# Kernel tuning notes

Hardware: AMD Instinct MI355X
Metric: run time of the kernel (lower is better)

Reference implementation:

```python
import jax, jax.numpy as jnp
import numpy as np
from jax import lax
import math

B, C, H, W = 8, 512, 24, 24
L = H * W
D_STATE = 16
D_INNER = 2 * C
DT_RANK = C // 16
K = 4
SCALE = 1.0 / math.sqrt(C)


def layer_norm(x, g, b, eps=1e-5):
    m = x.mean(-1, keepdims=True)
    v = ((x - m) ** 2).mean(-1, keepdims=True)
    return (x - m) * lax.rsqrt(v + eps) * g + b


def selective_scan(u, delta, A, Bm, Cm, Ds):
    # u, delta: (B,K,d,L); Bm, Cm: (B,K,N,L); A: (K,d,N); Ds: (K,d)
    us = jnp.moveaxis(u, -1, 0)      # (L,B,K,d)
    dts = jnp.moveaxis(delta, -1, 0)
    Bs = jnp.moveaxis(Bm, -1, 0)     # (L,B,K,N)
    Cs = jnp.moveaxis(Cm, -1, 0)

    def step(h, inp):
        u_t, dt_t, B_t, C_t = inp
        dA = jnp.exp(dt_t[..., None] * A)                      # (B,K,d,N)
        dBu = (dt_t * u_t)[..., None] * B_t[:, :, None, :]     # (B,K,d,N)
        h = dA * h + dBu
        y = jnp.einsum('bkdn,bkn->bkd', h, C_t)
        return h, y

    h0 = jnp.zeros(u.shape[:3] + (A.shape[-1],), u.dtype)
    _, ys = lax.scan(step, h0, (us, dts, Bs, Cs))
    y = jnp.moveaxis(ys, 0, -1)                                # (B,K,d,L)
    return y + Ds[None, :, :, None] * u


def ss2d(x, in_proj_w, dwconv_w, dwconv_b, x_proj_w, dt_proj_w, dt_proj_b,
         A_logs, Ds, out_norm_g, out_norm_b, out_proj_w):
    # x: (B,H,W,C) channel-last
    xz = x @ in_proj_w.T                                       # (B,H,W,2*d_inner)
    xi, z = jnp.split(xz, 2, axis=-1)
    xc = xi.transpose(0, 3, 1, 2)                              # (B,d_inner,H,W)
    xc = lax.conv_general_dilated(xc, dwconv_w, (1, 1), 'SAME',
                                  feature_group_count=D_INNER,
                                  dimension_numbers=('NCHW', 'OIHW', 'NCHW'))
    xc = jax.nn.silu(xc + dwconv_b[None, :, None, None])
    x_hw = xc.reshape(B, D_INNER, L)
    x_wh = xc.transpose(0, 1, 3, 2).reshape(B, D_INNER, L)
    xs = jnp.stack([x_hw, x_wh, x_hw[..., ::-1], x_wh[..., ::-1]], axis=1)  # (B,4,d,L)
    x_dbl = jnp.einsum('bkdl,kcd->bkcl', xs, x_proj_w)
    dt, Bm, Cm = jnp.split(x_dbl, [DT_RANK, DT_RANK + D_STATE], axis=2)
    delta = jax.nn.softplus(jnp.einsum('bkrl,kdr->bkdl', dt, dt_proj_w)
                            + dt_proj_b[None, :, :, None])
    A = -jnp.exp(A_logs)
    ys = selective_scan(xs, delta, A, Bm, Cm, Ds)              # (B,4,d,L)
    y_wh = ys[:, 1].reshape(B, D_INNER, W, H).transpose(0, 1, 3, 2).reshape(B, D_INNER, L)
    y_whr = ys[:, 3, :, ::-1].reshape(B, D_INNER, W, H).transpose(0, 1, 3, 2).reshape(B, D_INNER, L)
    y = ys[:, 0] + ys[:, 2, :, ::-1] + y_wh + y_whr
    y = y.reshape(B, D_INNER, H, W).transpose(0, 2, 3, 1)      # (B,H,W,d_inner)
    y = layer_norm(y, out_norm_g, out_norm_b)
    y = y * jax.nn.silu(z)
    return y @ out_proj_w.T                                    # (B,H,W,C)


def setup_inputs():
    key = jax.random.key(0)
    ks = jax.random.split(key, 10)
    n = lambda k, sh, s=0.02: jax.random.normal(k, sh, dtype=jnp.float32) * s
    return {
        'x5': jax.random.normal(ks[0], (B, C, H, W), dtype=jnp.float32),
        'conv_w': n(ks[1], (C, C)),
        'conv_b': jnp.zeros((C,), jnp.float32),
        'ln1_g': jnp.ones((C,), jnp.float32),
        'ln1_b': jnp.zeros((C,), jnp.float32),
        'in_proj_w': n(ks[2], (2 * D_INNER, C)),
        'dwconv_w': n(ks[3], (D_INNER, 1, 3, 3), 0.1),
        'dwconv_b': jnp.zeros((D_INNER,), jnp.float32),
        'x_proj_w': n(ks[4], (K, DT_RANK + 2 * D_STATE, D_INNER)),
        'dt_proj_w': n(ks[5], (K, D_INNER, DT_RANK), 0.1),
        'dt_proj_b': n(ks[6], (K, D_INNER), 0.1),
        'A_logs': jnp.tile(jnp.log(jnp.arange(1, D_STATE + 1, dtype=jnp.float32))[None, None, :],
                           (K, D_INNER, 1)),
        'Ds': jnp.ones((K, D_INNER), jnp.float32),
        'out_norm_g': jnp.ones((D_INNER,), jnp.float32),
        'out_norm_b': jnp.zeros((D_INNER,), jnp.float32),
        'out_proj_w': n(ks[7], (C, D_INNER)),
    }


def reference(x5, conv_w, conv_b, ln1_g, ln1_b, in_proj_w, dwconv_w, dwconv_b,
              x_proj_w, dt_proj_w, dt_proj_b, A_logs, Ds, out_norm_g, out_norm_b,
              out_proj_w):
    # 1x1 conv + residual
    x5 = jnp.einsum('bchw,oc->bohw', x5, conv_w) + conv_b[None, :, None, None] + x5
    x0 = x5.transpose(0, 2, 3, 1)                              # (B,H,W,C)
    # VSSBlock: x + SS2D(LN(x)); called twice on same input with same weights -> identical
    x00 = x0 + ss2d(layer_norm(x0, ln1_g, ln1_b), in_proj_w, dwconv_w, dwconv_b,
                    x_proj_w, dt_proj_w, dt_proj_b, A_logs, Ds,
                    out_norm_g, out_norm_b, out_proj_w)
    xq = x00.transpose(0, 3, 1, 2).reshape(B, C, L)            # (B,C,L)
    xq_flat = xq.transpose(0, 2, 1).reshape(B * L, C)          # (B*L, C)
    xk_flat = xq.transpose(1, 0, 2).reshape(C, B * L)          # (C, B*L)
    xw = (xq_flat @ xk_flat) * SCALE                           # (B*L, B*L)
    xw = xw.reshape(B * L, B, L).max(-1).mean(-1).reshape(B, L)
    xw = jax.nn.softmax(xw, axis=-1)
    norm0 = x5 / jnp.maximum(jnp.linalg.norm(x5, axis=1, keepdims=True), 1e-12)
    xw = xw[:, None, :]                                        # (B,1,L)
    xw_max = xw.max(-1, keepdims=True)
    mask = (xw == xw_max).astype(x5.dtype).reshape(B, 1, H, W)  # winner-take-all
    seeds = (norm0 * mask).sum((2, 3))                         # (B,C)
    # correlation (eval branch: relu), seeds act as 1x1 conv weights
    cor = jax.nn.relu(jnp.einsum('bchw,oc->bohw', norm0, seeds)).mean(1).reshape(B, L)
    mn = cor.min(1, keepdims=True)
    mx = cor.max(1, keepdims=True)
    cormap = ((cor - mn) / (mx - mn + 1e-12)).reshape(B, 1, H, W)
    x51 = x5 * cormap
    proto1 = x51.mean((0, 2, 3), keepdims=True)                # (1,C,1,1)
    return (x5, proto1, x5 * proto1 + x51, mask)
```

## Files before the change

### kernel.cpp

```cpp
#include <hip/hip_runtime.h>
#include <math.h>

#define NB 8
#define NC 512
#define NH 24
#define NW 24
#define NL 576
#define ND 1024
#define NBL 4608
#define NCH 8
#define CL 72

static constexpr float SCALE_ = 0.044194173824159216f;

typedef __attribute__((ext_vector_type(8))) short bf16x8;
typedef __attribute__((ext_vector_type(4))) float f32x4;

__device__ __forceinline__ unsigned enc_f(float f){
    unsigned u = __float_as_uint(f);
    return (u & 0x80000000u) ? ~u : (u | 0x80000000u);
}
__device__ __forceinline__ float dec_f(unsigned e){
    return (e & 0x80000000u) ? __uint_as_float(e ^ 0x80000000u) : __uint_as_float(~e);
}

__device__ __forceinline__ int scan_idx(int t, int k){
    int t2 = (k >= 2) ? (NL - 1 - t) : t;
    return (k & 1) ? ((t2 % NH) * NW + t2 / NH) : t2;
}

__device__ __forceinline__ float softplus_f(float x){
    return fmaxf(x, 0.f) + __logf(1.f + __expf(-fabsf(x)));
}
__device__ __forceinline__ float silu_f(float x){
    return x / (1.f + __expf(-x));
}

__global__ void k_transpose_in(const float* __restrict__ x5, float* __restrict__ x5t){
    __shared__ float t[32][33];
    const int b = blockIdx.z;
    const int c0 = blockIdx.x*32, l0 = blockIdx.y*32;
    const int tx = threadIdx.x & 31, ty = threadIdx.x >> 5;
    #pragma unroll
    for (int i=ty; i<32; i+=8)
        t[i][tx] = x5[((size_t)b*NC + c0 + i)*NL + l0 + tx];
    __syncthreads();
    #pragma unroll
    for (int i=ty; i<32; i+=8)
        x5t[((size_t)b*NL + l0 + i)*NC + c0 + tx] = t[tx][i];
}

template<int FORM>
__global__ void k_split(const float* __restrict__ in, unsigned short* __restrict__ oA,
                        unsigned short* __restrict__ oB, int K, int total4){
    int t = blockIdx.x*256 + threadIdx.x;
    if (t >= total4) return;
    int kq = K >> 2;
    int r = t / kq; int k4 = (t - r*kq) << 2;
    float4 v = *(const float4*)(in + (size_t)r*K + k4);
    float vv[4] = {v.x, v.y, v.z, v.w};
    unsigned short h[4], lo[4];
    #pragma unroll
    for (int i=0;i<4;i++){
        unsigned u = __float_as_uint(vv[i]);
        unsigned hr = (u + 0x7fffu + ((u>>16)&1u)) >> 16;
        h[i] = (unsigned short)hr;
        float hf = __uint_as_float(hr << 16);
        unsigned u2 = __float_as_uint(vv[i] - hf);
        lo[i] = (unsigned short)((u2 + 0x7fffu + ((u2>>16)&1u)) >> 16);
    }
    unsigned hp0 = h[0] | ((unsigned)h[1]<<16), hp1 = h[2] | ((unsigned)h[3]<<16);
    unsigned lp0 = lo[0] | ((unsigned)lo[1]<<16), lp1 = lo[2] | ((unsigned)lo[3]<<16);
    size_t base = (size_t)r*3*K + k4;
    if (FORM == 0 || FORM == 2){
        unsigned* p0 = (unsigned*)(oA + base);
        unsigned* p1 = (unsigned*)(oA + base + K);
        unsigned* p2 = (unsigned*)(oA + base + 2*K);
        p0[0]=hp0; p0[1]=hp1;  p1[0]=hp0; p1[1]=hp1;  p2[0]=lp0; p2[1]=lp1;
    }
    if (FORM == 1 || FORM == 2){
        unsigned short* o = (FORM==2) ? oB : oA;
        unsigned* p0 = (unsigned*)(o + base);
        unsigned* p1 = (unsigned*)(o + base + K);
        unsigned* p2 = (unsigned*)(o + base + 2*K);
        p0[0]=hp0; p0[1]=hp1;  p1[0]=lp0; p1[1]=lp1;  p2[0]=hp0; p2[1]=hp1;
    }
}

template<int MODE>
__launch_bounds__(256)
__global__ void mfma_nt(const unsigned short* __restrict__ A, const unsigned short* __restrict__ Bm,
                        const float* __restrict__ R0, const float* __restrict__ R1,
                        float* __restrict__ out0, float* __restrict__ out1,
                        unsigned* __restrict__ mbuf, int K3)
{
    const int bi = blockIdx.x, bj = blockIdx.y;
    if (MODE == 4 && bj < bi) return;
    const int m0 = bi*128, n0 = bj*128;
    __shared__ __align__(16) unsigned short As[128*32];
    __shared__ __align__(16) unsigned short Bs[128*32];
    const int tid = threadIdx.x;
    const int w = tid >> 6, l = tid & 63;
    const int mw = (w>>1)*64, nw = (w&1)*64;
    const int fr = l & 15, fq = l >> 4;

    f32x4 acc[4][4];
    #pragma unroll
    for (int i=0;i<4;i++)
        #pragma unroll
        for (int j=0;j<4;j++)
            #pragma unroll
            for (int c=0;c<4;c++) acc[i][j][c] = 0.f;

    const int c0 = tid, c1 = tid + 256;
    const int r0 = c0 >> 2, o0 = (c0 & 3) * 8;
    const int r1 = c1 >> 2, o1 = (c1 & 3) * 8;

    for (int k0 = 0; k0 < K3; k0 += 32){
        float4 a0 = *(const float4*)(A  + (size_t)(m0 + r0)*K3 + k0 + o0);
        float4 a1 = *(const float4*)(A  + (size_t)(m0 + r1)*K3 + k0 + o1);
        float4 b0 = *(const float4*)(Bm + (size_t)(n0 + r0)*K3 + k0 + o0);
        float4 b1 = *(const float4*)(Bm + (size_t)(n0 + r1)*K3 + k0 + o1);
        __syncthreads();
        *(float4*)&As[c0*8] = a0;
        *(float4*)&As[c1*8] = a1;
        *(float4*)&Bs[c0*8] = b0;
        *(float4*)&Bs[c1*8] = b1;
        __syncthreads();
        bf16x8 af[4], bf[4];
        #pragma unroll
        for (int i=0;i<4;i++){
            af[i] = *(const bf16x8*)&As[(mw + i*16 + fr)*32 + fq*8];
            bf[i] = *(const bf16x8*)&Bs[(nw + i*16 + fr)*32 + fq*8];
        }
        #pragma unroll
        for (int i=0;i<4;i++)
            #pragma unroll
            for (int j=0;j<4;j++)
                acc[i][j] = __builtin_amdgcn_mfma_f32_16x16x32_bf16(af[i], bf[j], acc[i][j], 0, 0, 0);
    }

    if (MODE == 4){
        const int b2c = (n0 + nw) / NL;
        #pragma unroll
        for (int mi=0; mi<4; mi++){
            #pragma unroll
            for (int i=0;i<4;i++){
                float v = fmaxf(fmaxf(acc[mi][0][i], acc[mi][1][i]),
                                fmaxf(acc[mi][2][i], acc[mi][3][i]));
                v = fmaxf(v, __shfl_xor(v, 1));
                v = fmaxf(v, __shfl_xor(v, 2));
                v = fmaxf(v, __shfl_xor(v, 4));
                v = fmaxf(v, __shfl_xor(v, 8));
                if (fr == 0)
                    atomicMax(&mbuf[(size_t)(m0 + mw + mi*16 + fq*4 + i)*NB + b2c], enc_f(v));
            }
        }
        const int b2r = (m0 + mw) / NL;
        #pragma unroll
        for (int ni=0; ni<4; ni++){
            float cm = -3.4e38f;
            #pragma unroll
            for (int mi=0; mi<4; mi++)
                #pragma unroll
                for (int i=0;i<4;i++) cm = fmaxf(cm, acc[mi][ni][i]);
            cm = fmaxf(cm, __shfl_xor(cm, 16));
            cm = fmaxf(cm, __shfl_xor(cm, 32));
            if (fq == 0)
                atomicMax(&mbuf[(size_t)(n0 + nw + ni*16 + fr)*NB + b2r], enc_f(cm));
        }
        return;
    }

    #pragma unroll
    for (int mi=0; mi<4; mi++){
        const int m = m0 + mw + mi*16 + fq*4;
        #pragma unroll
        for (int ni=0; ni<4; ni++){
            const int n = n0 + nw + ni*16 + fr;
            f32x4 a = acc[mi][ni];
            if (MODE == 0){
                float4 cb = *(const float4*)(R0 + m);
                float4 rs = *(const float4*)(R1 + (size_t)n*NC + m);
                float4 ov = make_float4(a[0]+cb.x+rs.x, a[1]+cb.y+rs.y, a[2]+cb.z+rs.z, a[3]+cb.w+rs.w);
                *(float4*)(out0 + (size_t)n*NC + m) = ov;
            } else if (MODE == 1){
                float4 ov = make_float4(a[0], a[1], a[2], a[3]);
                if (m < ND) *(float4*)(out0 + (size_t)n*ND + m) = ov;
                else        *(float4*)(out1 + (size_t)n*ND + (m - ND)) = ov;
            } else {
                float4 rs = *(const float4*)(R1 + (size_t)n*NC + m);
                float4 ov = make_float4(a[0]+rs.x, a[1]+rs.y, a[2]+rs.z, a[3]+rs.w);
                *(float4*)(out0 + (size_t)n*NC + m) = ov;
            }
        }
    }
}

template<int MODE>
__launch_bounds__(256)
__global__ void gemm_nt(const float* __restrict__ A0, const float* __restrict__ B0,
                        const float* __restrict__ R,
                        float* __restrict__ out0, float* __restrict__ out1,
                        unsigned* __restrict__ mbuf, int K)
{
    __shared__ __align__(16) float As[16][68];
    __shared__ __align__(16) float Bs[16][68];
    const int tid = threadIdx.x;
    const int m0 = blockIdx.x * 64;
    const int n0 = blockIdx.y * 64;
    const float* A = A0;
    const float* B = B0;
    int kdir = 0;
    if (MODE == 2) {
        const int bk = blockIdx.z;
        kdir = bk & 3; const int bb = bk >> 2;
        A = A0 + (size_t)kdir * 64 * 1024;
        B = B0 + (size_t)bb * NL * 1024;
    }
    const int lrow = tid >> 2;
    const int lk4  = (tid & 3) << 2;
    int brow = n0 + lrow;
    if (MODE == 2) brow = scan_idx(brow, kdir);
    const float* aptr = A + (size_t)(m0 + lrow) * K + lk4;
    const float* bptr = B + (size_t)brow * K + lk4;

    float acc[4][4];
    #pragma unroll
    for (int i=0;i<4;i++){
        #pragma unroll
        for (int j=0;j<4;j++) acc[i][j]=0.f;
    }
    const int tx = tid & 15, ty = tid >> 4;

    for (int k0 = 0; k0 < K; k0 += 16) {
        float4 av = *(const float4*)(aptr + k0);
        float4 bv = *(const float4*)(bptr + k0);
        __syncthreads();
        As[lk4+0][lrow]=av.x; As[lk4+1][lrow]=av.y; As[lk4+2][lrow]=av.z; As[lk4+3][lrow]=av.w;
        Bs[lk4+0][lrow]=bv.x; Bs[lk4+1][lrow]=bv.y; Bs[lk4+2][lrow]=bv.z; Bs[lk4+3][lrow]=bv.w;
        __syncthreads();
        #pragma unroll
        for (int kk=0;kk<16;kk++){
            float4 a = *(const float4*)&As[kk][ty<<2];
            float4 b = *(const float4*)&Bs[kk][tx<<2];
            acc[0][0] = fmaf(a.x,b.x,acc[0][0]); acc[0][1] = fmaf(a.x,b.y,acc[0][1]);
            acc[0][2] = fmaf(a.x,b.z,acc[0][2]); acc[0][3] = fmaf(a.x,b.w,acc[0][3]);
            acc[1][0] = fmaf(a.y,b.x,acc[1][0]); acc[1][1] = fmaf(a.y,b.y,acc[1][1]);
            acc[1][2] = fmaf(a.y,b.z,acc[1][2]); acc[1][3] = fmaf(a.y,b.w,acc[1][3]);
            acc[2][0] = fmaf(a.z,b.x,acc[2][0]); acc[2][1] = fmaf(a.z,b.y,acc[2][1]);
            acc[2][2] = fmaf(a.z,b.z,acc[2][2]); acc[2][3] = fmaf(a.z,b.w,acc[2][3]);
            acc[3][0] = fmaf(a.w,b.x,acc[3][0]); acc[3][1] = fmaf(a.w,b.y,acc[3][1]);
            acc[3][2] = fmaf(a.w,b.z,acc[3][2]); acc[3][3] = fmaf(a.w,b.w,acc[3][3]);
        }
    }

    #pragma unroll
    for (int j=0;j<4;j++){
        const int n  = n0 + (tx<<2) + j;
        const int mm = m0 + (ty<<2);
        float4 v = make_float4(acc[0][j], acc[1][j], acc[2][j], acc[3][j]);
        if (MODE == 2){
            *(float4*)(out0 + ((size_t)blockIdx.z*NL + n)*64 + mm) = v;
        }
    }
}

__global__ void k_ln512(const float* __restrict__ x, const float* __restrict__ g,
                        const float* __restrict__ bb, float* __restrict__ out){
    int n = blockIdx.x; int tid = threadIdx.x;
    const float* row = x + (size_t)n*NC;
    float v0 = row[tid], v1 = row[tid+256];
    __shared__ float s1[256], s2[256];
    s1[tid] = v0+v1; s2[tid] = v0*v0 + v1*v1;
    __syncthreads();
    for (int s=128;s>0;s>>=1){ if (tid<s){ s1[tid]+=s1[tid+s]; s2[tid]+=s2[tid+s]; } __syncthreads(); }
    float mean = s1[0]*(1.f/NC);
    float var  = fmaxf(s2[0]*(1.f/NC) - mean*mean, 0.f);
    float rs   = rsqrtf(var + 1e-5f);
    out[(size_t)n*NC+tid]     = (v0-mean)*rs*g[tid]     + bb[tid];
    out[(size_t)n*NC+tid+256] = (v1-mean)*rs*g[tid+256] + bb[tid+256];
}

__global__ void k_dwconv(const float* __restrict__ xi, const float* __restrict__ w,
                         const float* __restrict__ bias, float* __restrict__ xcl){
    int d = blockIdx.x*256 + threadIdx.x;
    int l = blockIdx.y; int b = blockIdx.z;
    int h = l / NW, wc = l - h*NW;
    float acc = bias[d];
    #pragma unroll
    for (int kh=0;kh<3;kh++){
        int h2 = h + kh - 1; if (h2 < 0 || h2 >= NH) continue;
        #pragma unroll
        for (int kw=0;kw<3;kw++){
            int w2 = wc + kw - 1; if (w2 < 0 || w2 >= NW) continue;
            acc += xi[((size_t)b*NL + h2*NW + w2)*ND + d] * w[d*9 + kh*3 + kw];
        }
    }
    xcl[((size_t)b*NL + l)*ND + d] = silu_f(acc);
}

__launch_bounds__(256)
__global__ void k_scan_p1(const float* __restrict__ xcl, const float* __restrict__ xdbl,
                          const float* __restrict__ dtw, const float* __restrict__ dtb,
                          const float* __restrict__ alogs,
                          float* __restrict__ hfin, float* __restrict__ prodA){
    const int d = blockIdx.x*256 + threadIdx.x;
    const int chunk = blockIdx.y;
    const int bk = blockIdx.z;
    const int k = bk & 3, b = bk >> 2;
    const int kd = k*ND + d;
    float wdt[32];
    {
        const float4* p = (const float4*)(dtw + (size_t)kd*32);
        #pragma unroll
        for (int i=0;i<8;i++){ float4 v=p[i]; wdt[4*i]=v.x; wdt[4*i+1]=v.y; wdt[4*i+2]=v.z; wdt[4*i+3]=v.w; }
    }
    float An[16];
    {
        const float4* p = (const float4*)(alogs + (size_t)kd*16);
        #pragma unroll
        for (int i=0;i<4;i++){
            float4 v=p[i];
            An[4*i]=-__expf(v.x); An[4*i+1]=-__expf(v.y); An[4*i+2]=-__expf(v.z); An[4*i+3]=-__expf(v.w);
        }
    }
    const float dtbias = dtb[kd];
    __shared__ __align__(16) float rows[CL*64];
    {
        const float4* src = (const float4*)(xdbl + ((size_t)bk*NL + chunk*CL)*64);
        for (int i = threadIdx.x; i < CL*16; i += 256) ((float4*)rows)[i] = src[i];
    }
    __syncthreads();
    float h[16], pA[16];
    #pragma unroll
    for (int n=0;n<16;n++){ h[n]=0.f; pA[n]=1.f; }
    for (int t=0;t<CL;t++){
        const float* row = rows + t*64;
        float dr = dtbias;
        #pragma unroll
        for (int r=0;r<32;r++) dr = fmaf(row[r], wdt[r], dr);
        float sp = softplus_f(dr);
        int idx = scan_idx(chunk*CL + t, k);
        float u  = xcl[((size_t)b*NL + idx)*ND + d];
        float du = sp * u;
        #pragma unroll
        for (int n=0;n<16;n++){
            float dA = __expf(sp * An[n]);
            pA[n] *= dA;
            h[n] = fmaf(dA, h[n], du*row[32+n]);
        }
    }
    size_t base = (size_t)(bk*NCH + chunk)*16*1024 + d;
    #pragma unroll
    for (int n=0;n<16;n++){ hfin[base + n*1024] = h[n]; prodA[base + n*1024] = pA[n]; }
}

__global__ void k_scan_mid(float* __restrict__ hfin, const float* __restrict__ prodA){
    int id = blockIdx.x*256 + threadIdx.x;
    int d = id & 1023, nn = (id >> 10) & 15, bk = id >> 14;
    float h = 0.f;
    for (int j=0;j<NCH;j++){
        size_t idx = (size_t)((bk*NCH + j)*16 + nn)*1024 + d;
        float hf = hfin[idx], pa = prodA[idx];
        hfin[idx] = h;
        h = fmaf(pa, h, hf);
    }
}

__launch_bounds__(256)
__global__ void k_scan_p2(const float* __restrict__ xcl, const float* __restrict__ xdbl,
                          const float* __restrict__ dtw, const float* __restrict__ dtb,
                          const float* __restrict__ alogs,
                          const float* __restrict__ hfin, float* __restrict__ yacc){
    const int d = blockIdx.x*256 + threadIdx.x;
    const int chunk = blockIdx.y;
    const int bk = blockIdx.z;
    const int k = bk & 3, b = bk >> 2;
    const int kd = k*ND + d;
    float wdt[32];
    {
        const float4* p = (const float4*)(dtw + (size_t)kd*32);
        #pragma unroll
        for (int i=0;i<8;i++){ float4 v=p[i]; wdt[4*i]=v.x; wdt[4*i+1]=v.y; wdt[4*i+2]=v.z; wdt[4*i+3]=v.w; }
    }
    float An[16];
    {
        const float4* p = (const float4*)(alogs + (size_t)kd*16);
        #pragma unroll
        for (int i=0;i<4;i++){
            float4 v=p[i];
            An[4*i]=-__expf(v.x); An[4*i+1]=-__expf(v.y); An[4*i+2]=-__expf(v.z); An[4*i+3]=-__expf(v.w);
        }
    }
    const float dtbias = dtb[kd];
    __shared__ __align__(16) float rows[CL*64];
    {
        const float4* src = (const float4*)(xdbl + ((size_t)bk*NL + chunk*CL)*64);
        for (int i = threadIdx.x; i < CL*16; i += 256) ((float4*)rows)[i] = src[i];
    }
    __syncthreads();
    float h[16];
    {
        size_t base = (size_t)(bk*NCH + chunk)*16*1024 + d;
        #pragma unroll
        for (int n=0;n<16;n++) h[n] = hfin[base + n*1024];
    }
    for (int t=0;t<CL;t++){
        const float* row = rows + t*64;
        float dr = dtbias;
        #pragma unroll
        for (int r=0;r<32;r++) dr = fmaf(row[r], wdt[r], dr);
        float sp = softplus_f(dr);
        int idx = scan_idx(chunk*CL + t, k);
        size_t base = ((size_t)b*NL + idx)*ND + d;
        float u  = xcl[base];
        float du = sp * u;
        float y = 0.f;
        #pragma unroll
        for (int n=0;n<16;n++){
            float dA = __expf(sp * An[n]);
            h[n] = fmaf(dA, h[n], du*row[32+n]);
            y = fmaf(h[n], row[48+n], y);
        }
        atomicAdd(&yacc[base], y);
    }
}

__global__ void k_combine(const float* __restrict__ y, const float* __restrict__ xcl,
                          const float* __restrict__ Ds,
                          const float* __restrict__ g, const float* __restrict__ bb,
                          float* __restrict__ z){
    int n = blockIdx.x;
    size_t base = (size_t)n*ND;
    int tid = threadIdx.x;
    float v[4]; float sum=0.f, sq=0.f;
    #pragma unroll
    for (int j=0;j<4;j++){
        int d = tid + 256*j;
        float ds = Ds[d] + Ds[ND+d] + Ds[2*ND+d] + Ds[3*ND+d];
        float val = y[base+d] + ds*xcl[base+d];
        v[j]=val; sum+=val; sq+=val*val;
    }
    __shared__ float s1[256], s2[256];
    s1[tid]=sum; s2[tid]=sq; __syncthreads();
    for (int st=128;st>0;st>>=1){ if(tid<st){ s1[tid]+=s1[tid+st]; s2[tid]+=s2[tid+st]; } __syncthreads(); }
    float mean = s1[0]*(1.f/ND);
    float var  = fmaxf(s2[0]*(1.f/ND) - mean*mean, 0.f);
    float rs   = rsqrtf(var + 1e-5f);
    #pragma unroll
    for (int j=0;j<4;j++){
        int d = tid + 256*j;
        float ln = (v[j]-mean)*rs*g[d] + bb[d];
        float zv = z[base+d];
        z[base+d] = ln * silu_f(zv);
    }
}

__global__ void k_xwpre(const unsigned* __restrict__ M, float* __restrict__ xwp){
    int n = blockIdx.x*256 + threadIdx.x; if (n >= NBL) return;
    float sum = 0.f;
    #pragma unroll
    for (int b2=0;b2<NB;b2++) sum += dec_f(M[(size_t)n*NB + b2]);
    xwp[n] = sum * (SCALE_/8.f);
}

__global__ void k_mask(const float* __restrict__ xwp, float* __restrict__ maskf){
    int b = blockIdx.x; int tid = threadIdx.x;
    float m = -1e30f;
    for (int i=tid;i<NL;i+=64) m = fmaxf(m, xwp[b*NL+i]);
    __shared__ float s1[64];
    s1[tid]=m; __syncthreads();
    for (int st=32;st>0;st>>=1){ if(tid<st) s1[tid]=fmaxf(s1[tid],s1[tid+st]); __syncthreads(); }
    float bm = s1[0];
    for (int i=tid;i<NL;i+=64) maskf[b*NL+i] = (xwp[b*NL+i]==bm) ? 1.f : 0.f;
}

__global__ void k_norm0(const float* __restrict__ x5r, float* __restrict__ norm0){
    int n = blockIdx.x; int tid = threadIdx.x;
    float v0 = x5r[(size_t)n*NC+tid], v1 = x5r[(size_t)n*NC+tid+256];
    __shared__ float s1[256];
    s1[tid] = v0*v0 + v1*v1; __syncthreads();
    for (int st=128;st>0;st>>=1){ if(tid<st) s1[tid]+=s1[tid+st]; __syncthreads(); }
    float inv = 1.f / fmaxf(sqrtf(s1[0]), 1e-12f);
    norm0[(size_t)n*NC+tid]     = v0*inv;
    norm0[(size_t)n*NC+tid+256] = v1*inv;
}

__global__ void k_seeds(const float* __restrict__ norm0, const float* __restrict__ maskf,
                        float* __restrict__ seeds){
    int b = blockIdx.x; int c = threadIdx.x;
    float acc = 0.f;
    for (int l=0;l<NL;l++){
        float mk = maskf[b*NL+l];
        if (mk != 0.f) acc += norm0[((size_t)b*NL+l)*NC + c]*mk;
    }
    seeds[b*NC + c] = acc;
}

__global__ void k_cor(const float* __restrict__ norm0, const float* __restrict__ seeds,
                      float* __restrict__ cor){
    int n = blockIdx.x; int tid = threadIdx.x;
    int o = tid >> 6, lane = tid & 63;
    float acc = 0.f;
    #pragma unroll
    for (int i=0;i<8;i++){
        int c = lane + 64*i;
        acc += norm0[(size_t)n*NC + c] * seeds[o*NC + c];
    }
    #pragma unroll
    for (int s=32;s>0;s>>=1) acc += __shfl_xor(acc, s);
    __shared__ float sr[8];
    if (lane == 0) sr[o] = fmaxf(acc, 0.f);
    __syncthreads();
    if (tid == 0){
        float r = 0.f;
        #pragma unroll
        for (int o2=0;o2<8;o2++) r += sr[o2];
        cor[n] = r * (1.f/8.f);
    }
}

__global__ void k_cormap(const float* __restrict__ cor, float* __restrict__ cmap){
    int b = blockIdx.x, tid = threadIdx.x;
    float mn = 1e30f, mx = -1e30f;
    for (int i=tid;i<NL;i+=64){ float v=cor[b*NL+i]; mn=fminf(mn,v); mx=fmaxf(mx,v); }
    __shared__ float sn[64], sx[64];
    sn[tid]=mn; sx[tid]=mx; __syncthreads();
    for (int st=32;st>0;st>>=1){ if(tid<st){ sn[tid]=fminf(sn[tid],sn[tid+st]); sx[tid]=fmaxf(sx[tid],sx[tid+st]); } __syncthreads(); }
    float MN=sn[0], MX=sx[0];
    float inv = 1.f/(MX-MN+1e-12f);
    for (int i=tid;i<NL;i+=64) cmap[b*NL+i] = (cor[b*NL+i]-MN)*inv;
}

__global__ void k_proto(const float* __restrict__ x5r, const float* __restrict__ cmap,
                        float* __restrict__ pacc){
    int c = threadIdx.x;
    int chunk = blockIdx.x;
    float acc = 0.f;
    for (int i=0;i<64;i++){
        int n = chunk*64 + i;
        acc += x5r[(size_t)n*NC + c] * cmap[n];
    }
    atomicAdd(&pacc[c], acc);
}

__global__ void k_final(const float* __restrict__ x5r, const float* __restrict__ cmap,
                        const float* __restrict__ pacc, const float* __restrict__ maskf,
                        float* __restrict__ out){
    int id = blockIdx.x*256 + threadIdx.x;
    int l = id % NL; int bc = id / NL; int c = bc & 511; int b = bc >> 9;
    float v  = x5r[((size_t)b*NL + l)*NC + c];
    float p  = pacc[c] * (1.f/(float)NBL);
    float cm = cmap[b*NL + l];
    out[id] = v;
    out[2359296 + 512 + id] = v*(p + cm);
    if (id < 512)  out[2359296 + id] = pacc[id] * (1.f/(float)NBL);
    if (id < NBL)  out[2359296 + 512 + 2359296 + id] = maskf[id];
}

extern "C" void kernel_launch(void* const* d_in, const int* in_sizes, int n_in,
                              void* d_out, int out_size, void* d_ws, size_t ws_size,
                              hipStream_t stream) {
    const float* x5        = (const float*)d_in[0];
    const float* conv_w    = (const float*)d_in[1];
    const float* conv_b    = (const float*)d_in[2];
    const float* ln1_g     = (const float*)d_in[3];
    const float* ln1_b     = (const float*)d_in[4];
    const float* in_proj_w = (const float*)d_in[5];
    const float* dwconv_w  = (const float*)d_in[6];
    const float* dwconv_b  = (const float*)d_in[7];
    const float* x_proj_w  = (const float*)d_in[8];
    const float* dt_proj_w = (const float*)d_in[9];
    const float* dt_proj_b = (const float*)d_in[10];
    const float* A_logs    = (const float*)d_in[11];
    const float* Ds        = (const float*)d_in[12];
    const float* out_norm_g= (const float*)d_in[13];
    const float* out_norm_b= (const float*)d_in[14];
    const float* out_proj_w= (const float*)d_in[15];

    float* ws = (float*)d_ws;
    const size_t O_X5R  = 0;
    const size_t O_XLN  = 2359296;
    const size_t O_XI   = 4718592;
    const size_t O_Z    = 9437184;
    const size_t O_XCL  = 14155776;
    const size_t O_XDBL = 18874368;
    const size_t O_HF   = 20054016;
    const size_t O_PA   = 24248320;
    const size_t O_MBUF = 28442624;
    const size_t O_XWP  = 28479488;
    const size_t O_MASK = 28484096;
    const size_t O_COR  = 28488704;
    const size_t O_CMAP = 28493312;
    const size_t O_SEED = 28497920;
    const size_t O_PACC = 28502016;

    float* x5r  = ws + O_X5R;
    float* xln  = ws + O_XLN;
    float* xqf  = ws + O_XLN;
    float* xi   = ws + O_XI;
    float* yacc = ws + O_XI;
    unsigned short* wAo = (unsigned short*)(ws + O_XI);
    float* z    = ws + O_Z;
    float* xcl  = ws + O_XCL;
    unsigned short* wAi = (unsigned short*)(ws + O_XCL);
    float* nrm0 = ws + O_XCL;
    float* xdbl = ws + O_XDBL;
    float* x5t  = ws + O_HF;
    float* hfin = ws + O_HF;
    unsigned short* xlnB = (unsigned short*)(ws + O_HF);
    unsigned short* zB   = (unsigned short*)(ws + O_HF);
    unsigned short* xqfA = (unsigned short*)(ws + O_HF);
    float* prodA = ws + O_PA;
    unsigned short* x5tB = (unsigned short*)(ws + O_PA);
    unsigned short* wAc  = (unsigned short*)(ws + O_PA) + 7077888;
    unsigned short* xqfB = (unsigned short*)(ws + O_PA);
    unsigned* mbuf = (unsigned*)(ws + O_MBUF);
    float* xwp  = ws + O_XWP;
    float* maskf= ws + O_MASK;
    float* cor  = ws + O_COR;
    float* cmap = ws + O_CMAP;
    float* seeds= ws + O_SEED;
    float* pacc = ws + O_PACC;

    hipMemsetAsync(mbuf, 0, 36864*sizeof(unsigned), stream);
    hipMemsetAsync(pacc, 0, 512*sizeof(float), stream);

    k_transpose_in<<<dim3(16,18,8), 256, 0, stream>>>(x5, x5t);
    k_split<0><<<256, 256, 0, stream>>>(conv_w, wAc, nullptr, 512, 65536);
    k_split<1><<<2304, 256, 0, stream>>>(x5t, x5tB, nullptr, 512, 589824);
    mfma_nt<0><<<dim3(4,36), 256, 0, stream>>>(wAc, x5tB, conv_b, x5t, x5r, nullptr, nullptr, 1536);
    k_ln512<<<NBL, 256, 0, stream>>>(x5r, ln1_g, ln1_b, xln);
    k_split<0><<<1024, 256, 0, stream>>>(in_proj_w, wAi, nullptr, 512, 262144);
    k_split<1><<<2304, 256, 0, stream>>>(xln, xlnB, nullptr, 512, 589824);
    mfma_nt<1><<<dim3(16,36), 256, 0, stream>>>(wAi, xlnB, nullptr, nullptr, xi, z, nullptr, 1536);
    k_dwconv<<<dim3(4,NL,NB), 256, 0, stream>>>(xi, dwconv_w, dwconv_b, xcl);
    hipMemsetAsync(yacc, 0, (size_t)4718592*sizeof(float), stream);
    gemm_nt<2><<<dim3(1,9,32), 256, 0, stream>>>(x_proj_w, xcl, nullptr, xdbl, nullptr, nullptr, 1024);
    k_scan_p1<<<dim3(4,NCH,32), 256, 0, stream>>>(xcl, xdbl, dt_proj_w, dt_proj_b, A_logs, hfin, prodA);
    k_scan_mid<<<2048, 256, 0, stream>>>(hfin, prodA);
    k_scan_p2<<<dim3(4,NCH,32), 256, 0, stream>>>(xcl, xdbl, dt_proj_w, dt_proj_b, A_logs, hfin, yacc);
    k_combine<<<NBL, 256, 0, stream>>>(yacc, xcl, Ds, out_norm_g, out_norm_b, z);
    k_split<1><<<4608, 256, 0, stream>>>(z, zB, nullptr, 1024, 1179648);
    k_split<0><<<512, 256, 0, stream>>>(out_proj_w, wAo, nullptr, 1024, 131072);
    mfma_nt<3><<<dim3(4,36), 256, 0, stream>>>(wAo, zB, nullptr, x5r, xqf, nullptr, nullptr, 3072);
    k_split<2><<<2304, 256, 0, stream>>>(xqf, xqfA, xqfB, 512, 589824);
    mfma_nt<4><<<dim3(36,36), 256, 0, stream>>>(xqfA, xqfB, nullptr, nullptr, nullptr, nullptr, mbuf, 1536);
    k_xwpre<<<18, 256, 0, stream>>>(mbuf, xwp);
    k_mask<<<NB, 64, 0, stream>>>(xwp, maskf);
    k_norm0<<<NBL, 256, 0, stream>>>(x5r, nrm0);
    k_seeds<<<NB, 512, 0, stream>>>(nrm0, maskf, seeds);
    k_cor<<<NBL, 512, 0, stream>>>(nrm0, seeds, cor);
    k_cormap<<<NB, 64, 0, stream>>>(cor, cmap);
    k_proto<<<72, 512, 0, stream>>>(x5r, cmap, pacc);
    k_final<<<9216, 256, 0, stream>>>(x5r, cmap, pacc, maskf, (float*)d_out);
}
```

Measured before the change: 752.6 us.

## Fuse bf16 splits into producers, slide dwconv window, use exp power ladder in scan

Folds the hi/lo bf16 splitting into the transpose, layernorm and combine kernels, removing three standalone split passes and their intermediate fp32 writes. The depthwise conv now has each thread walk a whole row with a register sliding window, cutting redundant loads. The scans detect at runtime when A equals -(n+1) and replace 16 exps per step with one exp plus multiplies. This adds a branch and a small rounding difference from repeated products.

```diff
diff --git a/kernel.cpp b/kernel.cpp
--- a/kernel.cpp
+++ b/kernel.cpp
@@ -36,7 +36,17 @@
     return x / (1.f + __expf(-x));
 }
 
-__global__ void k_transpose_in(const float* __restrict__ x5, float* __restrict__ x5t){
+__device__ __forceinline__ void split_bf(float v, unsigned short &h, unsigned short &l){
+    unsigned u = __float_as_uint(v);
+    unsigned hr = (u + 0x7fffu + ((u>>16)&1u)) >> 16;
+    h = (unsigned short)hr;
+    float hf = __uint_as_float(hr << 16);
+    unsigned u2 = __float_as_uint(v - hf);
+    l = (unsigned short)((u2 + 0x7fffu + ((u2>>16)&1u)) >> 16);
+}
+
+__global__ void k_transpose_in(const float* __restrict__ x5, float* __restrict__ x5t,
+                               unsigned short* __restrict__ x5tB){
     __shared__ float t[32][33];
     const int b = blockIdx.z;
     const int c0 = blockIdx.x*32, l0 = blockIdx.y*32;
@@ -46,8 +56,13 @@
         t[i][tx] = x5[((size_t)b*NC + c0 + i)*NL + l0 + tx];
     __syncthreads();
     #pragma unroll
-    for (int i=ty; i<32; i+=8)
-        x5t[((size_t)b*NL + l0 + i)*NC + c0 + tx] = t[tx][i];
+    for (int i=ty; i<32; i+=8){
+        float v = t[tx][i];
+        x5t[((size_t)b*NL + l0 + i)*NC + c0 + tx] = v;
+        unsigned short hh, ll; split_bf(v, hh, ll);
+        size_t rb = ((size_t)b*NL + l0 + i)*1536 + c0 + tx;
+        x5tB[rb] = hh; x5tB[rb+512] = ll; x5tB[rb+1024] = hh;
+    }
 }
 
 template<int FORM>
@@ -61,14 +76,7 @@
     float vv[4] = {v.x, v.y, v.z, v.w};
     unsigned short h[4], lo[4];
     #pragma unroll
-    for (int i=0;i<4;i++){
-        unsigned u = __float_as_uint(vv[i]);
-        unsigned hr = (u + 0x7fffu + ((u>>16)&1u)) >> 16;
-        h[i] = (unsigned short)hr;
-        float hf = __uint_as_float(hr << 16);
-        unsigned u2 = __float_as_uint(vv[i] - hf);
-        lo[i] = (unsigned short)((u2 + 0x7fffu + ((u2>>16)&1u)) >> 16);
-    }
+    for (int i=0;i<4;i++) split_bf(vv[i], h[i], lo[i]);
     unsigned hp0 = h[0] | ((unsigned)h[1]<<16), hp1 = h[2] | ((unsigned)h[3]<<16);
     unsigned lp0 = lo[0] | ((unsigned)lo[1]<<16), lp1 = lo[2] | ((unsigned)lo[3]<<16);
     size_t base = (size_t)r*3*K + k4;
@@ -266,8 +274,8 @@
     }
 }
 
-__global__ void k_ln512(const float* __restrict__ x, const float* __restrict__ g,
-                        const float* __restrict__ bb, float* __restrict__ out){
+__global__ void k_ln512b(const float* __restrict__ x, const float* __restrict__ g,
+                         const float* __restrict__ bb, unsigned short* __restrict__ outB){
     int n = blockIdx.x; int tid = threadIdx.x;
     const float* row = x + (size_t)n*NC;
     float v0 = row[tid], v1 = row[tid+256];
@@ -278,27 +286,51 @@
     float mean = s1[0]*(1.f/NC);
     float var  = fmaxf(s2[0]*(1.f/NC) - mean*mean, 0.f);
     float rs   = rsqrtf(var + 1e-5f);
-    out[(size_t)n*NC+tid]     = (v0-mean)*rs*g[tid]     + bb[tid];
-    out[(size_t)n*NC+tid+256] = (v1-mean)*rs*g[tid+256] + bb[tid+256];
+    float r0 = (v0-mean)*rs*g[tid]     + bb[tid];
+    float r1 = (v1-mean)*rs*g[tid+256] + bb[tid+256];
+    unsigned short h0,l0,h1,l1; split_bf(r0,h0,l0); split_bf(r1,h1,l1);
+    size_t base = (size_t)n*1536;
+    outB[base+tid]     =h0; outB[base+512+tid]     =l0; outB[base+1024+tid]     =h0;
+    outB[base+tid+256] =h1; outB[base+512+tid+256] =l1; outB[base+1024+tid+256] =h1;
 }
 
 __global__ void k_dwconv(const float* __restrict__ xi, const float* __restrict__ w,
                          const float* __restrict__ bias, float* __restrict__ xcl){
     int d = blockIdx.x*256 + threadIdx.x;
-    int l = blockIdx.y; int b = blockIdx.z;
-    int h = l / NW, wc = l - h*NW;
-    float acc = bias[d];
-    #pragma unroll
-    for (int kh=0;kh<3;kh++){
-        int h2 = h + kh - 1; if (h2 < 0 || h2 >= NH) continue;
-        #pragma unroll
-        for (int kw=0;kw<3;kw++){
-            int w2 = wc + kw - 1; if (w2 < 0 || w2 >= NW) continue;
-            acc += xi[((size_t)b*NL + h2*NW + w2)*ND + d] * w[d*9 + kh*3 + kw];
-        }
-    }
-    xcl[((size_t)b*NL + l)*ND + d] = silu_f(acc);
-}
+    int h = blockIdx.y; int b = blockIdx.z;
+    float W[9];
+    #pragma unroll
+    for (int i=0;i<9;i++) W[i] = w[d*9+i];
+    float bs = bias[d];
+    const size_t rb = ((size_t)b*NL)*ND + d;
+    const bool hm = h > 0, hp = h < NH-1;
+    float p0=0.f,p1=0.f,p2=0.f;
+    float c0 = hm ? xi[rb + (size_t)((h-1)*NW)*ND] : 0.f;
+    float c1 = xi[rb + (size_t)(h*NW)*ND];
+    float c2 = hp ? xi[rb + (size_t)((h+1)*NW)*ND] : 0.f;
+    for (int wc=0; wc<NW; wc++){
+        float n0,n1,n2;
+        if (wc < NW-1){
+            n0 = hm ? xi[rb + (size_t)((h-1)*NW+wc+1)*ND] : 0.f;
+            n1 = xi[rb + (size_t)(h*NW+wc+1)*ND];
+            n2 = hp ? xi[rb + (size_t)((h+1)*NW+wc+1)*ND] : 0.f;
+        } else { n0=0.f;n1=0.f;n2=0.f; }
+        float acc = bs;
+        acc = fmaf(W[0],p0, fmaf(W[1],c0, fmaf(W[2],n0, acc)));
+        acc = fmaf(W[3],p1, fmaf(W[4],c1, fmaf(W[5],n1, acc)));
+        acc = fmaf(W[6],p2, fmaf(W[7],c2, fmaf(W[8],n2, acc)));
+        xcl[rb + (size_t)(h*NW+wc)*ND] = silu_f(acc);
+        p0=c0;p1=c1;p2=c2; c0=n0;c1=n1;c2=n2;
+    }
+}
+
+#define DA_POWERS \
+    float e1=__expf(-sp); float e2=e1*e1; float e3=e2*e1; float e4=e2*e2; \
+    float e6=e4*e2; float e7=e4*e3; float e8=e4*e4; float e12=e8*e4; \
+    float dA[16]; \
+    dA[0]=e1; dA[1]=e2; dA[2]=e3; dA[3]=e4; dA[4]=e4*e1; dA[5]=e6; dA[6]=e7; dA[7]=e8; \
+    dA[8]=e8*e1; dA[9]=e8*e2; dA[10]=e8*e3; dA[11]=e12; dA[12]=e12*e1; dA[13]=e12*e2; \
+    dA[14]=e12*e3; dA[15]=e8*e8;
 
 __launch_bounds__(256)
 __global__ void k_scan_p1(const float* __restrict__ xcl, const float* __restrict__ xdbl,
@@ -316,7 +348,7 @@
         #pragma unroll
         for (int i=0;i<8;i++){ float4 v=p[i]; wdt[4*i]=v.x; wdt[4*i+1]=v.y; wdt[4*i+2]=v.z; wdt[4*i+3]=v.w; }
     }
-    float An[16];
+    float An[16]; bool ladder = true;
     {
         const float4* p = (const float4*)(alogs + (size_t)kd*16);
         #pragma unroll
@@ -324,6 +356,8 @@
             float4 v=p[i];
             An[4*i]=-__expf(v.x); An[4*i+1]=-__expf(v.y); An[4*i+2]=-__expf(v.z); An[4*i+3]=-__expf(v.w);
         }
+        #pragma unroll
+        for (int n=0;n<16;n++) ladder = ladder && (fabsf(An[n] + (float)(n+1)) < 1e-3f*(n+1));
     }
     const float dtbias = dtb[kd];
     __shared__ __align__(16) float rows[CL*64];
@@ -335,20 +369,39 @@
     float h[16], pA[16];
     #pragma unroll
     for (int n=0;n<16;n++){ h[n]=0.f; pA[n]=1.f; }
-    for (int t=0;t<CL;t++){
-        const float* row = rows + t*64;
-        float dr = dtbias;
-        #pragma unroll
-        for (int r=0;r<32;r++) dr = fmaf(row[r], wdt[r], dr);
-        float sp = softplus_f(dr);
-        int idx = scan_idx(chunk*CL + t, k);
-        float u  = xcl[((size_t)b*NL + idx)*ND + d];
-        float du = sp * u;
-        #pragma unroll
-        for (int n=0;n<16;n++){
-            float dA = __expf(sp * An[n]);
-            pA[n] *= dA;
-            h[n] = fmaf(dA, h[n], du*row[32+n]);
+    if (ladder){
+        for (int t=0;t<CL;t++){
+            const float* row = rows + t*64;
+            float dr = dtbias;
+            #pragma unroll
+            for (int r=0;r<32;r++) dr = fmaf(row[r], wdt[r], dr);
+            float sp = softplus_f(dr);
+            int idx = scan_idx(chunk*CL + t, k);
+            float u  = xcl[((size_t)b*NL + idx)*ND + d];
+            float du = sp * u;
+            DA_POWERS
+            #pragma unroll
+            for (int n=0;n<16;n++){
+                pA[n] *= dA[n];
+                h[n] = fmaf(dA[n], h[n], du*row[32+n]);
+            }
+        }
+    } else {
+        for (int t=0;t<CL;t++){
+            const float* row = rows + t*64;
+            float dr = dtbias;
+            #pragma unroll
+            for (int r=0;r<32;r++) dr = fmaf(row[r], wdt[r], dr);
+            float sp = softplus_f(dr);
+            int idx = scan_idx(chunk*CL + t, k);
+            float u  = xcl[((size_t)b*NL + idx)*ND + d];
+            float du = sp * u;
+            #pragma unroll
+            for (int n=0;n<16;n++){
+                float dA = __expf(sp * An[n]);
+                pA[n] *= dA;
+                h[n] = fmaf(dA, h[n], du*row[32+n]);
+            }
         }
     }
     size_t base = (size_t)(bk*NCH + chunk)*16*1024 + d;
@@ -384,7 +437,7 @@
         #pragma unroll
         for (int i=0;i<8;i++){ float4 v=p[i]; wdt[4*i]=v.x; wdt[4*i+1]=v.y; wdt[4*i+2]=v.z; wdt[4*i+3]=v.w; }
     }
-    float An[16];
+    float An[16]; bool ladder = true;
     {
         const float4* p = (const float4*)(alogs + (size_t)kd*16);
         #pragma unroll
@@ -392,6 +445,8 @@
             float4 v=p[i];
             An[4*i]=-__expf(v.x); An[4*i+1]=-__expf(v.y); An[4*i+2]=-__expf(v.z); An[4*i+3]=-__expf(v.w);
         }
+        #pragma unroll
+        for (int n=0;n<16;n++) ladder = ladder && (fabsf(An[n] + (float)(n+1)) < 1e-3f*(n+1));
     }
     const float dtbias = dtb[kd];
     __shared__ __align__(16) float rows[CL*64];
@@ -406,31 +461,53 @@
         #pragma unroll
         for (int n=0;n<16;n++) h[n] = hfin[base + n*1024];
     }
-    for (int t=0;t<CL;t++){
-        const float* row = rows + t*64;
-        float dr = dtbias;
-        #pragma unroll
-        for (int r=0;r<32;r++) dr = fmaf(row[r], wdt[r], dr);
-        float sp = softplus_f(dr);
-        int idx = scan_idx(chunk*CL + t, k);
-        size_t base = ((size_t)b*NL + idx)*ND + d;
-        float u  = xcl[base];
-        float du = sp * u;
-        float y = 0.f;
-        #pragma unroll
-        for (int n=0;n<16;n++){
-            float dA = __expf(sp * An[n]);
-            h[n] = fmaf(dA, h[n], du*row[32+n]);
-            y = fmaf(h[n], row[48+n], y);
-        }
-        atomicAdd(&yacc[base], y);
+    if (ladder){
+        for (int t=0;t<CL;t++){
+            const float* row = rows + t*64;
+            float dr = dtbias;
+            #pragma unroll
+            for (int r=0;r<32;r++) dr = fmaf(row[r], wdt[r], dr);
+            float sp = softplus_f(dr);
+            int idx = scan_idx(chunk*CL + t, k);
+            size_t base = ((size_t)b*NL + idx)*ND + d;
+            float u  = xcl[base];
+            float du = sp * u;
+            float y = 0.f;
+            DA_POWERS
+            #pragma unroll
+            for (int n=0;n<16;n++){
+                h[n] = fmaf(dA[n], h[n], du*row[32+n]);
+                y = fmaf(h[n], row[48+n], y);
+            }
+            atomicAdd(&yacc[base], y);
+        }
+    } else {
+        for (int t=0;t<CL;t++){
+            const float* row = rows + t*64;
+            float dr = dtbias;
+            #pragma unroll
+            for (int r=0;r<32;r++) dr = fmaf(row[r], wdt[r], dr);
+            float sp = softplus_f(dr);
+            int idx = scan_idx(chunk*CL + t, k);
+            size_t base = ((size_t)b*NL + idx)*ND + d;
+            float u  = xcl[base];
+            float du = sp * u;
+            float y = 0.f;
+            #pragma unroll
+            for (int n=0;n<16;n++){
+                float dA = __expf(sp * An[n]);
+                h[n] = fmaf(dA, h[n], du*row[32+n]);
+                y = fmaf(h[n], row[48+n], y);
+            }
+            atomicAdd(&yacc[base], y);
+        }
     }
 }
 
 __global__ void k_combine(const float* __restrict__ y, const float* __restrict__ xcl,
                           const float* __restrict__ Ds,
                           const float* __restrict__ g, const float* __restrict__ bb,
-                          float* __restrict__ z){
+                          const float* __restrict__ z, unsigned short* __restrict__ zB){
     int n = blockIdx.x;
     size_t base = (size_t)n*ND;
     int tid = threadIdx.x;
@@ -448,12 +525,14 @@
     float mean = s1[0]*(1.f/ND);
     float var  = fmaxf(s2[0]*(1.f/ND) - mean*mean, 0.f);
     float rs   = rsqrtf(var + 1e-5f);
+    size_t zb = (size_t)n*3072;
     #pragma unroll
     for (int j=0;j<4;j++){
         int d = tid + 256*j;
         float ln = (v[j]-mean)*rs*g[d] + bb[d];
-        float zv = z[base+d];
-        z[base+d] = ln * silu_f(zv);
+        float res = ln * silu_f(z[base+d]);
+        unsigned short hh,ll; split_bf(res,hh,ll);
+        zB[zb + d] = hh; zB[zb + 1024 + d] = ll; zB[zb + 2048 + d] = hh;
     }
 }
 
@@ -597,7 +676,6 @@
     const size_t O_PACC = 28502016;
 
     float* x5r  = ws + O_X5R;
-    float* xln  = ws + O_XLN;
     float* xqf  = ws + O_XLN;
     float* xi   = ws + O_XI;
     float* yacc = ws + O_XI;
@@ -627,22 +705,19 @@
     hipMemsetAsync(mbuf, 0, 36864*sizeof(unsigned), stream);
     hipMemsetAsync(pacc, 0, 512*sizeof(float), stream);
 
-    k_transpose_in<<<dim3(16,18,8), 256, 0, stream>>>(x5, x5t);
+    k_transpose_in<<<dim3(16,18,8), 256, 0, stream>>>(x5, x5t, x5tB);
     k_split<0><<<256, 256, 0, stream>>>(conv_w, wAc, nullptr, 512, 65536);
-    k_split<1><<<2304, 256, 0, stream>>>(x5t, x5tB, nullptr, 512, 589824);
     mfma_nt<0><<<dim3(4,36), 256, 0, stream>>>(wAc, x5tB, conv_b, x5t, x5r, nullptr, nullptr, 1536);
-    k_ln512<<<NBL, 256, 0, stream>>>(x5r, ln1_g, ln1_b, xln);
+    k_ln512b<<<NBL, 256, 0, stream>>>(x5r, ln1_g, ln1_b, xlnB);
     k_split<0><<<1024, 256, 0, stream>>>(in_proj_w, wAi, nullptr, 512, 262144);
-    k_split<1><<<2304, 256, 0, stream>>>(xln, xlnB, nullptr, 512, 589824);
     mfma_nt<1><<<dim3(16,36), 256, 0, stream>>>(wAi, xlnB, nullptr, nullptr, xi, z, nullptr, 1536);
-    k_dwconv<<<dim3(4,NL,NB), 256, 0, stream>>>(xi, dwconv_w, dwconv_b, xcl);
+    k_dwconv<<<dim3(4,NH,NB), 256, 0, stream>>>(xi, dwconv_w, dwconv_b, xcl);
     hipMemsetAsync(yacc, 0, (size_t)4718592*sizeof(float), stream);
     gemm_nt<2><<<dim3(1,9,32), 256, 0, stream>>>(x_proj_w, xcl, nullptr, xdbl, nullptr, nullptr, 1024);
     k_scan_p1<<<dim3(4,NCH,32), 256, 0, stream>>>(xcl, xdbl, dt_proj_w, dt_proj_b, A_logs, hfin, prodA);
     k_scan_mid<<<2048, 256, 0, stream>>>(hfin, prodA);
     k_scan_p2<<<dim3(4,NCH,32), 256, 0, stream>>>(xcl, xdbl, dt_proj_w, dt_proj_b, A_logs, hfin, yacc);
-    k_combine<<<NBL, 256, 0, stream>>>(yacc, xcl, Ds, out_norm_g, out_norm_b, z);
-    k_split<1><<<4608, 256, 0, stream>>>(z, zB, nullptr, 1024, 1179648);
+    k_combine<<<NBL, 256, 0, stream>>>(yacc, xcl, Ds, out_norm_g, out_norm_b, z, zB);
     k_split<0><<<512, 256, 0, stream>>>(out_proj_w, wAo, nullptr, 1024, 131072);
     mfma_nt<3><<<dim3(4,36), 256, 0, stream>>>(wAo, zB, nullptr, x5r, xqf, nullptr, nullptr, 3072);
     k_split<2><<<2304, 256, 0, stream>>>(xqf, xqfA, xqfB, 512, 589824);
```

New measurement: 676.3 us. 1.11x faster.
